# Kernel optimization log

Hardware: AMD Instinct MI355X
Metric: run time of the kernel (lower is better)

Reference implementation:

```python
import jax, jax.numpy as jnp
import numpy as np

KERNEL_MUL = 2.0
KERNEL_NUM = 5
FIX_SIGMA = None


def setup_inputs() -> dict:
    key = jax.random.key(0)
    k1, k2 = jax.random.split(key)
    source = jax.random.normal(k1, (4096, 512), dtype=jnp.float32)
    target = jax.random.normal(k2, (4096, 512), dtype=jnp.float32)
    return {"source": source, "target": target}


def reference(source, target):
    batch_size = source.shape[0]
    total = jnp.concatenate([source, target], axis=0)  # [N, D], N = n1 + n2
    n_samples = total.shape[0]

    # Pairwise squared L2 distances via Gram-matrix trick (same math as
    # the explicit NxNxD broadcast in the original, without materializing it).
    sq = jnp.sum(total * total, axis=1)               # [N]
    gram = total @ total.T                            # [N, N]
    l2 = sq[:, None] + sq[None, :] - 2.0 * gram       # [N, N]

    if FIX_SIGMA:
        bandwidth = jnp.asarray(FIX_SIGMA, dtype=l2.dtype)
    else:
        # torch used L2_distance.data -> no gradient through bandwidth
        bandwidth = jax.lax.stop_gradient(jnp.sum(l2)) / (n_samples ** 2 - n_samples)
    bandwidth = bandwidth / (KERNEL_MUL ** (KERNEL_NUM // 2))

    # Multi-bandwidth Gaussian kernel sum
    kernels = jnp.zeros_like(l2)
    for i in range(KERNEL_NUM):
        kernels = kernels + jnp.exp(-l2 / (bandwidth * (KERNEL_MUL ** i)))

    b = batch_size
    XX = kernels[:b, :b]
    YY = kernels[b:, b:]
    XY = kernels[:b, b:]
    YX = kernels[b:, :b]
    loss = jnp.mean(XX + YY - XY - YX)
    return loss
```

## Files before the change

kernel.cpp:

```cpp
#include <hip/hip_runtime.h>
#include <math.h>

typedef float f32x4 __attribute__((ext_vector_type(4)));
typedef int   i32x4 __attribute__((ext_vector_type(4)));
typedef signed char i8x8 __attribute__((ext_vector_type(8)));

#define NROWS 8192
#define NCOLS 512
#define BHALF 4096
#define NT    64
#define NBLK  2080
#define CSPART 256
#define QS    24.0f
#define INV_S2 (1.0f / (24.0f * 24.0f))

__global__ void k_conv(const float* __restrict__ src, const float* __restrict__ tgt,
                       signed char* __restrict__ bfrag, float* __restrict__ sq,
                       int* __restrict__ sqi, float* __restrict__ cspart) {
    __shared__ signed char ldsc[32][528];
    __shared__ float colp[4][NCOLS];
    int t = threadIdx.x, w = t >> 6, l = t & 63;
    int r0 = blockIdx.x * 32;
    float c0x=0.f,c0y=0.f,c0z=0.f,c0w=0.f, c1x=0.f,c1y=0.f,c1z=0.f,c1w=0.f;
    #pragma unroll
    for (int r = 0; r < 8; ++r) {
        int row = r0 + w * 8 + r;
        const float* base = (row < BHALF) ? (src + (size_t)row * NCOLS)
                                          : (tgt + (size_t)(row - BHALF) * NCOLS);
        float4 a = ((const float4*)base)[2 * l];
        float4 b = ((const float4*)base)[2 * l + 1];
        int q0 = (int)rintf(fminf(fmaxf(a.x * QS, -127.f), 127.f));
        int q1 = (int)rintf(fminf(fmaxf(a.y * QS, -127.f), 127.f));
        int q2 = (int)rintf(fminf(fmaxf(a.z * QS, -127.f), 127.f));
        int q3 = (int)rintf(fminf(fmaxf(a.w * QS, -127.f), 127.f));
        int q4 = (int)rintf(fminf(fmaxf(b.x * QS, -127.f), 127.f));
        int q5 = (int)rintf(fminf(fmaxf(b.y * QS, -127.f), 127.f));
        int q6 = (int)rintf(fminf(fmaxf(b.z * QS, -127.f), 127.f));
        int q7 = (int)rintf(fminf(fmaxf(b.w * QS, -127.f), 127.f));
        i8x8 v8;
        v8[0]=(signed char)q0; v8[1]=(signed char)q1; v8[2]=(signed char)q2; v8[3]=(signed char)q3;
        v8[4]=(signed char)q4; v8[5]=(signed char)q5; v8[6]=(signed char)q6; v8[7]=(signed char)q7;
        *(i8x8*)&ldsc[w * 8 + r][l * 8] = v8;
        float s = a.x*a.x + a.y*a.y + a.z*a.z + a.w*a.w
                + b.x*b.x + b.y*b.y + b.z*b.z + b.w*b.w;
        int si = q0*q0 + q1*q1 + q2*q2 + q3*q3 + q4*q4 + q5*q5 + q6*q6 + q7*q7;
        #pragma unroll
        for (int o = 32; o > 0; o >>= 1) {
            s  += __shfl_down(s, o);
            si += __shfl_down(si, o);
        }
        if (l == 0) { sq[row] = s; sqi[row] = si; }
        c0x += a.x; c0y += a.y; c0z += a.z; c0w += a.w;
        c1x += b.x; c1y += b.y; c1z += b.z; c1w += b.w;
    }
    colp[w][l*8+0] = c0x; colp[w][l*8+1] = c0y; colp[w][l*8+2] = c0z; colp[w][l*8+3] = c0w;
    colp[w][l*8+4] = c1x; colp[w][l*8+5] = c1y; colp[w][l*8+6] = c1z; colp[w][l*8+7] = c1w;
    __syncthreads();
    float s0 = colp[0][t] + colp[1][t] + colp[2][t] + colp[3][t];
    float s1 = colp[0][t+256] + colp[1][t+256] + colp[2][t+256] + colp[3][t+256];
    cspart[(size_t)blockIdx.x * NCOLS + t]       = s0;
    cspart[(size_t)blockIdx.x * NCOLS + t + 256] = s1;
    int rg0 = blockIdx.x * 2;
    #pragma unroll
    for (int c4 = 0; c4 < 4; ++c4) {
        int c = c4 * 256 + t;
        int g = c >> 9, sl = (c >> 4) & 31, lrr = c & 15;
        i32x4 v = *(const i32x4*)&ldsc[g * 16 + lrr][sl * 16];
        *(i32x4*)(bfrag + (size_t)(rg0 + g) * 8192 + sl * 256 + lrr * 16) = v;
    }
}

__global__ void k_bw(const float* __restrict__ sq, const float* __restrict__ cspart,
                     float* __restrict__ cvals) {
    __shared__ double red[1024];
    int t = threadIdx.x;
    double a = 0.0;
    #pragma unroll
    for (int i = 0; i < 8; ++i) a += (double)sq[t + i * 1024];
    red[t] = a; __syncthreads();
    for (int o = 512; o > 0; o >>= 1) { if (t < o) red[t] += red[t + o]; __syncthreads(); }
    double sT = red[0];
    __syncthreads();
    int c = t & 511, h = t >> 9;
    double d0 = 0.0, d1 = 0.0, d2 = 0.0, d3 = 0.0;
    int p0 = h * 128;
    #pragma unroll 8
    for (int p = 0; p < 128; p += 4) {
        d0 += (double)cspart[(size_t)(p0 + p + 0) * NCOLS + c];
        d1 += (double)cspart[(size_t)(p0 + p + 1) * NCOLS + c];
        d2 += (double)cspart[(size_t)(p0 + p + 2) * NCOLS + c];
        d3 += (double)cspart[(size_t)(p0 + p + 3) * NCOLS + c];
    }
    red[t] = (d0 + d1) + (d2 + d3);
    __syncthreads();
    double v = 0.0;
    if (t < 512) { double cs = red[t] + red[t + 512]; v = cs * cs; }
    __syncthreads();
    red[t] = v; __syncthreads();
    for (int o = 512; o > 0; o >>= 1) { if (t < o) red[t] += red[t + o]; __syncthreads(); }
    if (t == 0) {
        double G = red[0];
        double sum_l2 = 2.0 * (double)NROWS * sT - 2.0 * G;
        double denom = (double)NROWS * (double)NROWS - (double)NROWS;
        double bw = sum_l2 / denom / 4.0;
        const double L2E = 1.4426950408889634;
        double b = bw;
        #pragma unroll
        for (int k = 0; k < 5; ++k) { cvals[k] = (float)(L2E / b); b *= 2.0; }
    }
}

__global__ __launch_bounds__(256, 3)
void k_mmd(const signed char* __restrict__ bfrag, const int* __restrict__ sqi,
           const float* __restrict__ cvals, double* __restrict__ psum) {
    __shared__ float wred[4];

    int bid = blockIdx.x;
    int swz = (bid & 7) * (NBLK / 8) + (bid >> 3);
    int rem = swz;
    int I = 0;
    while (rem >= NT - I) { rem -= NT - I; ++I; }
    int J = I + rem;

    const int t  = threadIdx.x;
    const int w  = t >> 6;
    const int l  = t & 63;
    const int lr = l & 15;
    const int lk = l >> 4;

    const bool dsup = (I == J);
    int da, db;
    if (dsup) { da = (w == 2) ? 1 : 0; db = (w == 0) ? 0 : 1; }
    else      { da = w >> 1;           db = w & 1; }
    const int i_t = 2 * I + da, j_t = 2 * J + db;
    const int rowA0 = i_t * 64, rowB0 = j_t * 64;

    const int i_u = __builtin_amdgcn_readfirstlane(i_t);
    const int j_u = __builtin_amdgcn_readfirstlane(j_t);
    const signed char* bA = bfrag + (size_t)i_u * 32768;
    const signed char* bB = bfrag + (size_t)j_u * 32768;
    const int voff = lk * 256 + lr * 16;

    i32x4 acc[4][4] = {};
    #pragma unroll
    for (int kt = 0; kt < 8; ++kt) {
        i32x4 af[4], bf[4];
        #pragma unroll
        for (int m = 0; m < 4; ++m)
            af[m] = *(const i32x4*)(bA + m * 8192 + kt * 1024 + voff);
        #pragma unroll
        for (int n = 0; n < 4; ++n)
            bf[n] = *(const i32x4*)(bB + n * 8192 + kt * 1024 + voff);
        __builtin_amdgcn_s_setprio(1);
        #pragma unroll
        for (int m = 0; m < 4; ++m)
            #pragma unroll
            for (int n = 0; n < 4; ++n)
                acc[m][n] = __builtin_amdgcn_mfma_i32_16x16x64_i8(
                    af[m], bf[n], acc[m][n], 0, 0, 0);
        __builtin_amdgcn_s_setprio(0);
    }

    i32x4 sqa[4];
    #pragma unroll
    for (int m = 0; m < 4; ++m)
        sqa[m] = *(const i32x4*)&sqi[rowA0 + m * 16 + lk * 4];
    int sqb[4];
    #pragma unroll
    for (int n = 0; n < 4; ++n)
        sqb[n] = sqi[rowB0 + n * 16 + lr];
    float c4i = cvals[4] * INV_S2;

    const bool elem = dsup && ((w & 1) == 0);
    const float wb  = dsup ? 1.f : 2.f;
    const float sgn = ((rowA0 < BHALF) == (rowB0 < BHALF)) ? 1.f : -1.f;
    float local = 0.f;
    #pragma unroll
    for (int m = 0; m < 4; ++m)
        #pragma unroll
        for (int n = 0; n < 4; ++n)
            #pragma unroll
            for (int r = 0; r < 4; ++r) {
                int   d   = acc[m][n][r];
                int   l2i = sqa[m][r] + sqb[n] - 2 * d;
                float l2  = (float)l2i;
                float x  = exp2f(-l2 * c4i);
                float x2 = x * x;
                float x4 = x2 * x2;
                float x8 = x4 * x4;
                float e  = x + x2 + x4 + x8 + x8 * x8;
                if (elem) {
                    int gi = rowA0 + m * 16 + lk * 4 + r;
                    int gj = rowB0 + n * 16 + lr;
                    float wgt = (gj > gi) ? 2.f : ((gj == gi) ? 1.f : 0.f);
                    local += wgt * e;
                } else {
                    local += e;
                }
            }
    if (!elem) local *= wb * sgn;

    #pragma unroll
    for (int o = 32; o > 0; o >>= 1) local += __shfl_down(local, o);
    if (l == 0) wred[w] = local;
    __syncthreads();
    if (t == 0) {
        psum[blockIdx.x] = (double)((wred[0] + wred[1]) + (wred[2] + wred[3]));
    }
}

__global__ void k_final(const double* __restrict__ psum, float* __restrict__ out) {
    __shared__ double red[256];
    int t = threadIdx.x;
    double a = 0.0;
    for (int i = t; i < NBLK; i += 256) a += psum[i];
    red[t] = a; __syncthreads();
    for (int o = 128; o > 0; o >>= 1) { if (t < o) red[t] += red[t + o]; __syncthreads(); }
    if (t == 0) out[0] = (float)(red[0] * (1.0 / ((double)BHALF * (double)BHALF)));
}

extern "C" void kernel_launch(void* const* d_in, const int* in_sizes, int n_in,
                              void* d_out, int out_size, void* d_ws, size_t ws_size,
                              hipStream_t stream) {
    (void)in_sizes; (void)n_in; (void)out_size; (void)ws_size;
    const float* src = (const float*)d_in[0];
    const float* tgt = (const float*)d_in[1];
    float* out = (float*)d_out;
    char* ws = (char*)d_ws;
    signed char* bfrag = (signed char*)(ws);
    float*  sq     = (float*) (ws + 4194304);
    int*    sqi    = (int*)   (ws + 4194304 + 32768);
    float*  cspart = (float*) (ws + 4194304 + 65536);
    float*  cvals  = (float*) (ws + 4194304 + 65536 + 524288);
    double* psum   = (double*)(ws + 4194304 + 65536 + 524288 + 32);

    k_conv  <<<CSPART, 256, 0, stream>>>(src, tgt, bfrag, sq, sqi, cspart);
    k_bw    <<<1, 1024, 0, stream>>>(sq, cspart, cvals);
    k_mmd   <<<NBLK, 256, 0, stream>>>(bfrag, sqi, cvals, psum);
    k_final <<<1, 256, 0, stream>>>(psum, out);
}
```

Baseline: 64.98 us.

## Use single-wave 64x128 tiles over a triangular grid in MMD kernel

Each k_mmd block is now one wavefront computing a 64x128 tile of the Gram matrix, in place of a 4-wave block split into 64x64 sub-tiles. Blocks walk a triangular enumeration, with weighted handling of the diagonal tile. This raises the number of MFMAs per operand fragment loaded and drops the LDS reduction and barrier, but uses more accumulator registers per wave and may lower occupancy. It also switches to the raw exp2 intrinsic with an fma in the kernel sum, and widens the column-sum unrolling in k_bw.

```diff
diff --git a/kernel.cpp b/kernel.cpp
--- a/kernel.cpp
+++ b/kernel.cpp
@@ -8,8 +8,9 @@
 #define NROWS 8192
 #define NCOLS 512
 #define BHALF 4096
-#define NT    64
-#define NBLK  2080
+#define NTI   128
+#define NTJ   64
+#define NBLK  4160
 #define CSPART 256
 #define QS    24.0f
 #define INV_S2 (1.0f / (24.0f * 24.0f))
@@ -82,16 +83,20 @@
     double sT = red[0];
     __syncthreads();
     int c = t & 511, h = t >> 9;
-    double d0 = 0.0, d1 = 0.0, d2 = 0.0, d3 = 0.0;
+    double d0=0.0,d1=0.0,d2=0.0,d3=0.0,d4=0.0,d5=0.0,d6=0.0,d7=0.0;
     int p0 = h * 128;
-    #pragma unroll 8
-    for (int p = 0; p < 128; p += 4) {
+    #pragma unroll 4
+    for (int p = 0; p < 128; p += 8) {
         d0 += (double)cspart[(size_t)(p0 + p + 0) * NCOLS + c];
         d1 += (double)cspart[(size_t)(p0 + p + 1) * NCOLS + c];
         d2 += (double)cspart[(size_t)(p0 + p + 2) * NCOLS + c];
         d3 += (double)cspart[(size_t)(p0 + p + 3) * NCOLS + c];
-    }
-    red[t] = (d0 + d1) + (d2 + d3);
+        d4 += (double)cspart[(size_t)(p0 + p + 4) * NCOLS + c];
+        d5 += (double)cspart[(size_t)(p0 + p + 5) * NCOLS + c];
+        d6 += (double)cspart[(size_t)(p0 + p + 6) * NCOLS + c];
+        d7 += (double)cspart[(size_t)(p0 + p + 7) * NCOLS + c];
+    }
+    red[t] = ((d0 + d1) + (d2 + d3)) + ((d4 + d5) + (d6 + d7));
     __syncthreads();
     double v = 0.0;
     if (t < 512) { double cs = red[t] + red[t + 512]; v = cs * cs; }
@@ -110,103 +115,87 @@
     }
 }
 
-__global__ __launch_bounds__(256, 3)
+__global__ __launch_bounds__(64, 2)
 void k_mmd(const signed char* __restrict__ bfrag, const int* __restrict__ sqi,
            const float* __restrict__ cvals, double* __restrict__ psum) {
-    __shared__ float wred[4];
-
     int bid = blockIdx.x;
     int swz = (bid & 7) * (NBLK / 8) + (bid >> 3);
     int rem = swz;
     int I = 0;
-    while (rem >= NT - I) { rem -= NT - I; ++I; }
-    int J = I + rem;
-
-    const int t  = threadIdx.x;
-    const int w  = t >> 6;
-    const int l  = t & 63;
+    while (rem >= NTJ - (I >> 1)) { rem -= NTJ - (I >> 1); ++I; }
+    int J = (I >> 1) + rem;
+
+    const int l  = threadIdx.x;
     const int lr = l & 15;
     const int lk = l >> 4;
 
-    const bool dsup = (I == J);
-    int da, db;
-    if (dsup) { da = (w == 2) ? 1 : 0; db = (w == 0) ? 0 : 1; }
-    else      { da = w >> 1;           db = w & 1; }
-    const int i_t = 2 * I + da, j_t = 2 * J + db;
-    const int rowA0 = i_t * 64, rowB0 = j_t * 64;
-
-    const int i_u = __builtin_amdgcn_readfirstlane(i_t);
-    const int j_u = __builtin_amdgcn_readfirstlane(j_t);
+    const int rowA0 = I * 64, colB0 = J * 128;
+
+    const int i_u = __builtin_amdgcn_readfirstlane(I);
+    const int j_u = __builtin_amdgcn_readfirstlane(J);
     const signed char* bA = bfrag + (size_t)i_u * 32768;
-    const signed char* bB = bfrag + (size_t)j_u * 32768;
+    const signed char* bB = bfrag + (size_t)j_u * 65536;
     const int voff = lk * 256 + lr * 16;
 
-    i32x4 acc[4][4] = {};
+    i32x4 acc[4][8] = {};
     #pragma unroll
     for (int kt = 0; kt < 8; ++kt) {
-        i32x4 af[4], bf[4];
+        i32x4 af[4], bf[8];
         #pragma unroll
         for (int m = 0; m < 4; ++m)
             af[m] = *(const i32x4*)(bA + m * 8192 + kt * 1024 + voff);
         #pragma unroll
-        for (int n = 0; n < 4; ++n)
+        for (int n = 0; n < 8; ++n)
             bf[n] = *(const i32x4*)(bB + n * 8192 + kt * 1024 + voff);
-        __builtin_amdgcn_s_setprio(1);
         #pragma unroll
         for (int m = 0; m < 4; ++m)
             #pragma unroll
-            for (int n = 0; n < 4; ++n)
+            for (int n = 0; n < 8; ++n)
                 acc[m][n] = __builtin_amdgcn_mfma_i32_16x16x64_i8(
                     af[m], bf[n], acc[m][n], 0, 0, 0);
-        __builtin_amdgcn_s_setprio(0);
     }
 
     i32x4 sqa[4];
     #pragma unroll
     for (int m = 0; m < 4; ++m)
         sqa[m] = *(const i32x4*)&sqi[rowA0 + m * 16 + lk * 4];
-    int sqb[4];
-    #pragma unroll
-    for (int n = 0; n < 4; ++n)
-        sqb[n] = sqi[rowB0 + n * 16 + lr];
+    int sqb[8];
+    #pragma unroll
+    for (int n = 0; n < 8; ++n)
+        sqb[n] = sqi[colB0 + n * 16 + lr];
     float c4i = cvals[4] * INV_S2;
 
-    const bool elem = dsup && ((w & 1) == 0);
-    const float wb  = dsup ? 1.f : 2.f;
-    const float sgn = ((rowA0 < BHALF) == (rowB0 < BHALF)) ? 1.f : -1.f;
+    const bool diag = (J == (I >> 1));
+    const float sgn = ((rowA0 < BHALF) == (colB0 < BHALF)) ? 1.f : -1.f;
     float local = 0.f;
     #pragma unroll
     for (int m = 0; m < 4; ++m)
         #pragma unroll
-        for (int n = 0; n < 4; ++n)
+        for (int n = 0; n < 8; ++n)
             #pragma unroll
             for (int r = 0; r < 4; ++r) {
                 int   d   = acc[m][n][r];
                 int   l2i = sqa[m][r] + sqb[n] - 2 * d;
                 float l2  = (float)l2i;
-                float x  = exp2f(-l2 * c4i);
+                float x  = __builtin_amdgcn_exp2f(-l2 * c4i);
                 float x2 = x * x;
                 float x4 = x2 * x2;
                 float x8 = x4 * x4;
-                float e  = x + x2 + x4 + x8 + x8 * x8;
-                if (elem) {
+                float e  = fmaf(x8, x8, x8) + ((x + x2) + x4);
+                if (diag) {
                     int gi = rowA0 + m * 16 + lk * 4 + r;
-                    int gj = rowB0 + n * 16 + lr;
+                    int gj = colB0 + n * 16 + lr;
                     float wgt = (gj > gi) ? 2.f : ((gj == gi) ? 1.f : 0.f);
                     local += wgt * e;
                 } else {
                     local += e;
                 }
             }
-    if (!elem) local *= wb * sgn;
+    if (!diag) local *= 2.f * sgn;
 
     #pragma unroll
     for (int o = 32; o > 0; o >>= 1) local += __shfl_down(local, o);
-    if (l == 0) wred[w] = local;
-    __syncthreads();
-    if (t == 0) {
-        psum[blockIdx.x] = (double)((wred[0] + wred[1]) + (wred[2] + wred[3]));
-    }
+    if (l == 0) psum[blockIdx.x] = (double)local;
 }
 
 __global__ void k_final(const double* __restrict__ psum, float* __restrict__ out) {
@@ -236,6 +225,6 @@
 
     k_conv  <<<CSPART, 256, 0, stream>>>(src, tgt, bfrag, sq, sqi, cspart);
     k_bw    <<<1, 1024, 0, stream>>>(sq, cspart, cvals);
-    k_mmd   <<<NBLK, 256, 0, stream>>>(bfrag, sqi, cvals, psum);
+    k_mmd   <<<NBLK, 64, 0, stream>>>(bfrag, sqi, cvals, psum);
     k_final <<<1, 256, 0, stream>>>(psum, out);
 }
```

New measurement: 72.36 us. +11.4%, slower.
